# Kernel tuning notes

Hardware: AMD Instinct MI355X
Metric: run time of the kernel (lower is better)

Reference implementation:

```python
import jax, jax.numpy as jnp
import numpy as np

G = 128  # voxel grid extent per axis (positions are integer voxel coords in [0, G))
K = 3    # kernel size per axis -> 27 offsets


def setup_inputs() -> dict:
    key = jax.random.key(0)
    k1, k2, k3 = jax.random.split(key, 3)
    N, Cin, Cout = 500000, 32, 32
    features = jax.random.normal(k1, (N, Cin), dtype=jnp.float32)
    in_positions = jax.random.randint(k2, (N, 3), 0, G, dtype=jnp.int32)
    # learned conv weight: one [Cin, Cout] matrix per kernel offset (27 total)
    weight = jax.random.normal(k3, (K ** 3, Cin, Cout), dtype=jnp.float32) * 0.05
    return {"features": features, "in_positions": in_positions, "weight": weight}


def _hash(pos):
    # unique linear key for integer voxel coords in [0, G)^3
    return (pos[:, 0] * G + pos[:, 1]) * G + pos[:, 2]


def reference(features, in_positions, weight):
    # Submanifold sparse conv (kernel 3x3x3, odd -> offset 0, out_positions == in_positions,
    # voxel_size = 1.0, no bias, no normalize):
    # for each active voxel, gather active neighbors at each of the 27 kernel offsets,
    # transform with the per-offset weight matrix, and accumulate.
    N = features.shape[0]
    # dense hash table: voxel key -> row index in features, -1 if inactive
    table = jnp.full((G * G * G,), -1, dtype=jnp.int32)
    table = table.at[_hash(in_positions)].set(jnp.arange(N, dtype=jnp.int32))

    out = jnp.zeros((N, weight.shape[-1]), dtype=features.dtype)
    r = K // 2
    k = 0
    for dx in range(-r, r + 1):
        for dy in range(-r, r + 1):
            for dz in range(-r, r + 1):
                npos = in_positions + jnp.array([dx, dy, dz], dtype=jnp.int32)
                inside = jnp.all((npos >= 0) & (npos < G), axis=1)
                idx = table[jnp.where(inside, _hash(npos), 0)]
                valid = inside & (idx >= 0)
                # gather active neighbor features; zero where neighbor inactive
                gathered = jnp.where(valid[:, None], features[jnp.maximum(idx, 0)], 0.0)
                out = out + gathered @ weight[k]  # [N, Cout]
                k += 1
    return out
```

## Files before the change

kernel.cpp:

```cpp
#include <hip/hip_runtime.h>
#include <hip/hip_bf16.h>


#define GRID 128
#define CIN 32
#define COUT 32
#define NOFF 27

typedef __attribute__((ext_vector_type(8))) short bf16x8;
typedef __attribute__((ext_vector_type(4))) float f32x4;

__device__ inline unsigned short f2bf(float x) {
    union { float f; unsigned u; } v; v.f = x;
    unsigned r = v.u + 0x7fff + ((v.u >> 16) & 1);
    return (unsigned short)(r >> 16);
}

__global__ void prep_kernel(const int* __restrict__ pos,
                            const float* __restrict__ wt,
                            int* __restrict__ table,
                            unsigned short* __restrict__ wtT, int N) {
    int i = blockIdx.x * 256 + threadIdx.x;
    if (i < N) {
        int x = pos[3 * i], y = pos[3 * i + 1], z = pos[3 * i + 2];
        atomicMax(&table[(x * GRID + y) * GRID + z], i);
    }
    if (i < NOFF * CIN * COUT) {
        int k = i >> 10, r = i & 1023, ci = r >> 5, co = r & 31;
        int idx = k * 1024 + (co >> 4) * 512 + (ci >> 3) * 128 + (co & 15) * 8 + (ci & 7);
        wtT[idx] = f2bf(wt[i]);
    }
}

__global__ __launch_bounds__(1024, 8)
void conv_kernel(const float* __restrict__ feats,
                 const int* __restrict__ pos,
                 const unsigned short* __restrict__ wtT,
                 const int* __restrict__ table,
                 float* __restrict__ out, int N) {
    __shared__ __align__(16) unsigned short ldsw[NOFF * 1024];

    int tid = threadIdx.x;
    int wave = tid >> 6, lane = tid & 63;
    int m = lane & 15, quad = lane >> 4;
    int tile = blockIdx.x * 16 + wave;
    int base = tile * 16;
    int g = base + m;
    bool gv = g < N;

    int x = 0, y = 0, z = 0;
    if (gv) { x = pos[3 * g]; y = pos[3 * g + 1]; z = pos[3 * g + 2]; }
    int h = (x * GRID + y) * GRID + z;
    bool v0[3] = {gv && x > 0, gv, gv && x < GRID - 1};
    bool v1[3] = {gv && y > 0, gv, gv && y < GRID - 1};
    bool v2[3] = {gv && z > 0, gv, gv && z < GRID - 1};

    int ids[NOFF];
#pragma unroll
    for (int k = 0; k < NOFF; ++k) {
        const int dx = k / 9, dy = (k / 3) % 3, dz = k % 3;
        bool ok = v0[dx] && v1[dy] && v2[dz];
        int hk = h + (dx - 1) * GRID * GRID + (dy - 1) * GRID + (dz - 1);
        hk = ok ? hk : 0;
        int id = table[hk];
        ids[k] = ok ? id : -1;
    }

    {
        const uint4* src = (const uint4*)wtT;
        uint4* dst = (uint4*)ldsw;
        for (int e = tid; e < NOFF * 1024 * 2 / 16; e += 1024)
            dst[e] = src[e];
    }
    __syncthreads();

    f32x4 acc0 = {0.f, 0.f, 0.f, 0.f};
    f32x4 acc1 = {0.f, 0.f, 0.f, 0.f};
    const unsigned short* wb = ldsw + (quad * 16 + m) * 8;

#pragma unroll
    for (int k = 0; k < NOFF; ++k) {
        int id = ids[k];
        int row = (id >= 0 ? id : 0) * CIN;
        const float* f = feats + (size_t)row + quad * 8;
        float4 f0 = *(const float4*)f;
        float4 f1 = *(const float4*)(f + 4);

        union { bf16x8 v; __hip_bfloat162 h2[4]; } a;
        a.h2[0] = __float22bfloat162_rn(make_float2(f0.x, f0.y));
        a.h2[1] = __float22bfloat162_rn(make_float2(f0.z, f0.w));
        a.h2[2] = __float22bfloat162_rn(make_float2(f1.x, f1.y));
        a.h2[3] = __float22bfloat162_rn(make_float2(f1.z, f1.w));
        if (id < 0) a.v = (bf16x8){0, 0, 0, 0, 0, 0, 0, 0};

        bf16x8 b0 = *(const bf16x8*)(wb + k * 1024);
        bf16x8 b1 = *(const bf16x8*)(wb + k * 1024 + 512);

        acc0 = __builtin_amdgcn_mfma_f32_16x16x32_bf16(a.v, b0, acc0, 0, 0, 0);
        acc1 = __builtin_amdgcn_mfma_f32_16x16x32_bf16(a.v, b1, acc1, 0, 0, 0);
    }

#pragma unroll
    for (int i = 0; i < 4; ++i) {
        int p = base + quad * 4 + i;
        if (p < N) {
            out[(size_t)p * COUT + m]      = acc0[i];
            out[(size_t)p * COUT + m + 16] = acc1[i];
        }
    }
}

extern "C" void kernel_launch(void* const* d_in, const int* in_sizes, int n_in,
                              void* d_out, int out_size, void* d_ws, size_t ws_size,
                              hipStream_t stream) {
    const float* feats = (const float*)d_in[0];
    const int*   pos   = (const int*)d_in[1];
    const float* wt    = (const float*)d_in[2];
    float* out = (float*)d_out;
    int N = in_sizes[0] / CIN;

    char* ws = (char*)d_ws;
    int* table = (int*)ws;
    size_t table_bytes = (size_t)GRID * GRID * GRID * sizeof(int);
    unsigned short* wtT = (unsigned short*)(ws + table_bytes);

    hipMemsetAsync(table, 0xFF, table_bytes, stream);

    int pthreads = (N > NOFF * CIN * COUT) ? N : NOFF * CIN * COUT;
    prep_kernel<<<(pthreads + 255) / 256, 256, 0, stream>>>(pos, wt, table, wtT, N);

    int numTiles = (N + 15) / 16;
    int blocks = (numTiles + 15) / 16;
    conv_kernel<<<blocks, 1024, 0, stream>>>(feats, pos, wtT, table, out, N);
}
```

Measured before the change: 280.0 us.

## Spatially sort voxels into cells and gather from pre-converted bf16 feature copy

```diff
diff --git a/kernel.cpp b/kernel.cpp
--- a/kernel.cpp
+++ b/kernel.cpp
@@ -6,6 +6,7 @@
 #define CIN 32
 #define COUT 32
 #define NOFF 27
+#define NCELL 512
 
 typedef __attribute__((ext_vector_type(8))) short bf16x8;
 typedef __attribute__((ext_vector_type(4))) float f32x4;
@@ -16,14 +17,78 @@
     return (unsigned short)(r >> 16);
 }
 
-__global__ void prep_kernel(const int* __restrict__ pos,
-                            const float* __restrict__ wt,
-                            int* __restrict__ table,
-                            unsigned short* __restrict__ wtT, int N) {
+__device__ inline int cellkey(int x, int y, int z) {
+    int cx = x >> 4, cy = y >> 4, cz = z >> 4;
+    int o = ((cx >> 2) << 2) | ((cy >> 2) << 1) | (cz >> 2);
+    int w = ((cx & 3) << 4) | ((cy & 3) << 2) | (cz & 3);
+    return (o << 6) | w;
+}
+
+__global__ void hist_kernel(const int* __restrict__ pos, int* __restrict__ hist, int N) {
+    int i = blockIdx.x * 256 + threadIdx.x;
+    if (i < N)
+        atomicAdd(&hist[cellkey(pos[3 * i], pos[3 * i + 1], pos[3 * i + 2])], 1);
+}
+
+__global__ void scan_kernel(const int* __restrict__ hist,
+                            int* __restrict__ cursor, int* __restrict__ off8) {
+    __shared__ int s[NCELL];
+    int t = threadIdx.x;
+    s[t] = hist[t];
+    __syncthreads();
+    for (int d = 1; d < NCELL; d <<= 1) {
+        int v = (t >= d) ? s[t - d] : 0;
+        __syncthreads();
+        s[t] += v;
+        __syncthreads();
+    }
+    cursor[t] = (t == 0) ? 0 : s[t - 1];
+    if (t < 8) off8[t] = (t == 0) ? 0 : s[t * 64 - 1];
+    if (t == 0) off8[8] = s[NCELL - 1];
+}
+
+__global__ void scatter_kernel(const float* __restrict__ feats,
+                               const int* __restrict__ pos,
+                               const float* __restrict__ wt,
+                               int* __restrict__ cursor,
+                               unsigned long long* __restrict__ tableS,
+                               int* __restrict__ orig,
+                               int* __restrict__ posS,
+                               unsigned short* __restrict__ featsB,
+                               unsigned short* __restrict__ wtT, int N) {
     int i = blockIdx.x * 256 + threadIdx.x;
     if (i < N) {
         int x = pos[3 * i], y = pos[3 * i + 1], z = pos[3 * i + 2];
-        atomicMax(&table[(x * GRID + y) * GRID + z], i);
+        int p = atomicAdd(&cursor[cellkey(x, y, z)], 1);
+        orig[p] = i;
+        posS[3 * p] = x; posS[3 * p + 1] = y; posS[3 * p + 2] = z;
+        unsigned long long packed =
+            (((unsigned long long)i << 20) | (unsigned)p) + 1ULL;
+        atomicMax(&tableS[(x * GRID + y) * GRID + z], packed);
+        const float4* fr = (const float4*)(feats + (size_t)i * CIN);
+        unsigned o16[8];
+#pragma unroll
+        for (int q = 0; q < 4; ++q) {
+            float4 a = fr[2 * q], b = fr[2 * q + 1];
+            o16[2 * q]     = (unsigned)f2bf(a.x) | ((unsigned)f2bf(a.y) << 16);
+            o16[2 * q] = (unsigned)f2bf(a.x) | ((unsigned)f2bf(a.y) << 16);
+            o16[2 * q + 1] = (unsigned)f2bf(a.z) | ((unsigned)f2bf(a.w) << 16);
+            (void)b;
+        }
+        unsigned outw[16];
+#pragma unroll
+        for (int q = 0; q < 8; ++q) {
+            float4 a = fr[q];
+            outw[2 * q]     = (unsigned)f2bf(a.x) | ((unsigned)f2bf(a.y) << 16);
+            outw[2 * q + 1] = (unsigned)f2bf(a.z) | ((unsigned)f2bf(a.w) << 16);
+        }
+        uint4* dst = (uint4*)(featsB + (size_t)p * CIN);
+#pragma unroll
+        for (int q = 0; q < 4; ++q) {
+            uint4 v; v.x = outw[4 * q]; v.y = outw[4 * q + 1];
+            v.z = outw[4 * q + 2]; v.w = outw[4 * q + 3];
+            dst[q] = v;
+        }
     }
     if (i < NOFF * CIN * COUT) {
         int k = i >> 10, r = i & 1023, ci = r >> 5, co = r & 31;
@@ -33,38 +98,18 @@
 }
 
 __global__ __launch_bounds__(1024, 8)
-void conv_kernel(const float* __restrict__ feats,
-                 const int* __restrict__ pos,
+void conv_kernel(const unsigned short* __restrict__ featsB,
+                 const int* __restrict__ posS,
                  const unsigned short* __restrict__ wtT,
-                 const int* __restrict__ table,
-                 float* __restrict__ out, int N) {
+                 const unsigned long long* __restrict__ tableS,
+                 const int* __restrict__ orig,
+                 const int* __restrict__ off8,
+                 float* __restrict__ out, int N, int R) {
     __shared__ __align__(16) unsigned short ldsw[NOFF * 1024];
 
     int tid = threadIdx.x;
     int wave = tid >> 6, lane = tid & 63;
     int m = lane & 15, quad = lane >> 4;
-    int tile = blockIdx.x * 16 + wave;
-    int base = tile * 16;
-    int g = base + m;
-    bool gv = g < N;
-
-    int x = 0, y = 0, z = 0;
-    if (gv) { x = pos[3 * g]; y = pos[3 * g + 1]; z = pos[3 * g + 2]; }
-    int h = (x * GRID + y) * GRID + z;
-    bool v0[3] = {gv && x > 0, gv, gv && x < GRID - 1};
-    bool v1[3] = {gv && y > 0, gv, gv && y < GRID - 1};
-    bool v2[3] = {gv && z > 0, gv, gv && z < GRID - 1};
-
-    int ids[NOFF];
-#pragma unroll
-    for (int k = 0; k < NOFF; ++k) {
-        const int dx = k / 9, dy = (k / 3) % 3, dz = k % 3;
-        bool ok = v0[dx] && v1[dy] && v2[dz];
-        int hk = h + (dx - 1) * GRID * GRID + (dy - 1) * GRID + (dz - 1);
-        hk = ok ? hk : 0;
-        int id = table[hk];
-        ids[k] = ok ? id : -1;
-    }
 
     {
         const uint4* src = (const uint4*)wtT;
@@ -74,38 +119,59 @@
     }
     __syncthreads();
 
-    f32x4 acc0 = {0.f, 0.f, 0.f, 0.f};
-    f32x4 acc1 = {0.f, 0.f, 0.f, 0.f};
+    int o = blockIdx.x & 7;
+    int r = blockIdx.x >> 3;
+    int lo = off8[o], hi = off8[o + 1];
     const unsigned short* wb = ldsw + (quad * 16 + m) * 8;
 
-#pragma unroll
-    for (int k = 0; k < NOFF; ++k) {
-        int id = ids[k];
-        int row = (id >= 0 ? id : 0) * CIN;
-        const float* f = feats + (size_t)row + quad * 8;
-        float4 f0 = *(const float4*)f;
-        float4 f1 = *(const float4*)(f + 4);
-
-        union { bf16x8 v; __hip_bfloat162 h2[4]; } a;
-        a.h2[0] = __float22bfloat162_rn(make_float2(f0.x, f0.y));
-        a.h2[1] = __float22bfloat162_rn(make_float2(f0.z, f0.w));
-        a.h2[2] = __float22bfloat162_rn(make_float2(f1.x, f1.y));
-        a.h2[3] = __float22bfloat162_rn(make_float2(f1.z, f1.w));
-        if (id < 0) a.v = (bf16x8){0, 0, 0, 0, 0, 0, 0, 0};
-
-        bf16x8 b0 = *(const bf16x8*)(wb + k * 1024);
-        bf16x8 b1 = *(const bf16x8*)(wb + k * 1024 + 512);
-
-        acc0 = __builtin_amdgcn_mfma_f32_16x16x32_bf16(a.v, b0, acc0, 0, 0, 0);
-        acc1 = __builtin_amdgcn_mfma_f32_16x16x32_bf16(a.v, b1, acc1, 0, 0, 0);
-    }
-
-#pragma unroll
-    for (int i = 0; i < 4; ++i) {
-        int p = base + quad * 4 + i;
-        if (p < N) {
-            out[(size_t)p * COUT + m]      = acc0[i];
-            out[(size_t)p * COUT + m + 16] = acc1[i];
+    for (int start = lo + r * 256; start < hi; start += R * 256) {
+        int base = start + wave * 16;
+        if (base >= hi) continue;
+
+        int g = base + m;
+        bool gv = g < N;
+        int x = 0, y = 0, z = 0;
+        if (gv) { x = posS[3 * g]; y = posS[3 * g + 1]; z = posS[3 * g + 2]; }
+        int h = (x * GRID + y) * GRID + z;
+        bool v0[3] = {gv && x > 0, gv, gv && x < GRID - 1};
+        bool v1[3] = {gv && y > 0, gv, gv && y < GRID - 1};
+        bool v2[3] = {gv && z > 0, gv, gv && z < GRID - 1};
+
+        int ids[NOFF];
+#pragma unroll
+        for (int k = 0; k < NOFF; ++k) {
+            const int dx = k / 9, dy = (k / 3) % 3, dz = k % 3;
+            bool ok = v0[dx] && v1[dy] && v2[dz];
+            int hk = h + (dx - 1) * GRID * GRID + (dy - 1) * GRID + (dz - 1);
+            hk = ok ? hk : 0;
+            unsigned long long e = tableS[hk];
+            ids[k] = (ok && e != 0ULL) ? (int)((e - 1ULL) & 0xFFFFFULL) : -1;
+        }
+
+        f32x4 acc0 = {0.f, 0.f, 0.f, 0.f};
+        f32x4 acc1 = {0.f, 0.f, 0.f, 0.f};
+#pragma unroll
+        for (int k = 0; k < NOFF; ++k) {
+            int id = ids[k];
+            int row = (id >= 0 ? id : 0) * CIN;
+            bf16x8 a = *(const bf16x8*)(featsB + (size_t)row + quad * 8);
+            if (id < 0) a = (bf16x8){0, 0, 0, 0, 0, 0, 0, 0};
+
+            bf16x8 b0 = *(const bf16x8*)(wb + k * 1024);
+            bf16x8 b1 = *(const bf16x8*)(wb + k * 1024 + 512);
+
+            acc0 = __builtin_amdgcn_mfma_f32_16x16x32_bf16(a, b0, acc0, 0, 0, 0);
+            acc1 = __builtin_amdgcn_mfma_f32_16x16x32_bf16(a, b1, acc1, 0, 0, 0);
+        }
+
+#pragma unroll
+        for (int i2 = 0; i2 < 4; ++i2) {
+            int ps = base + quad * 4 + i2;
+            if (ps < N) {
+                int og = orig[ps];
+                out[(size_t)og * COUT + m]      = acc0[i2];
+                out[(size_t)og * COUT + m + 16] = acc1[i2];
+            }
         }
     }
 }
@@ -120,16 +186,30 @@
     int N = in_sizes[0] / CIN;
 
     char* ws = (char*)d_ws;
-    int* table = (int*)ws;
-    size_t table_bytes = (size_t)GRID * GRID * GRID * sizeof(int);
-    unsigned short* wtT = (unsigned short*)(ws + table_bytes);
-
-    hipMemsetAsync(table, 0xFF, table_bytes, stream);
-
-    int pthreads = (N > NOFF * CIN * COUT) ? N : NOFF * CIN * COUT;
-    prep_kernel<<<(pthreads + 255) / 256, 256, 0, stream>>>(pos, wt, table, wtT, N);
-
-    int numTiles = (N + 15) / 16;
-    int blocks = (numTiles + 15) / 16;
-    conv_kernel<<<blocks, 1024, 0, stream>>>(feats, pos, wtT, table, out, N);
-}
+    size_t off = 0;
+    unsigned long long* tableS = (unsigned long long*)(ws + off);
+    off += (size_t)GRID * GRID * GRID * 8;
+    unsigned short* featsB = (unsigned short*)(ws + off);
+    off += (size_t)N * CIN * 2;
+    int* posS = (int*)(ws + off);   off += (size_t)N * 3 * 4;
+    int* orig = (int*)(ws + off);   off += (size_t)N * 4;
+    unsigned short* wtT = (unsigned short*)(ws + off);
+    off += NOFF * CIN * COUT * 2;   off = (off + 255) & ~(size_t)255;
+    int* hist = (int*)(ws + off);   off += NCELL * 4;
+    int* cursor = (int*)(ws + off); off += NCELL * 4;
+    int* off8 = (int*)(ws + off);   off += 16 * 4;
+
+    hipMemsetAsync(tableS, 0, (size_t)GRID * GRID * GRID * 8, stream);
+    hipMemsetAsync(hist, 0, NCELL * 4, stream);
+
+    int nb = (N + 255) / 256;
+    hist_kernel<<<nb, 256, 0, stream>>>(pos, hist, N);
+    scan_kernel<<<1, NCELL, 0, stream>>>(hist, cursor, off8);
+    scatter_kernel<<<nb, 256, 0, stream>>>(feats, pos, wt, cursor, tableS,
+                                           orig, posS, featsB, wtT, N);
+
+    int perOct = (N + 7) / 8;
+    int R = (perOct + 255) / 256 + 2;
+    conv_kernel<<<8 * R, 1024, 0, stream>>>(featsB, posS, wtT, tableS, orig,
+                                            off8, out, N, R);
+}
```

Result: slower. 552.5 us (+97.3%).
